# Kernel optimization log

Hardware: AMD Instinct MI355X
Metric: run time of the kernel (lower is better)

The kernel has to match this reference:

```python
import jax, jax.numpy as jnp
import numpy as np

D_CAT = 4096   # number of multinomial categories (input_dim)
HID = 256      # hidden_dim
B = 4096       # batch_size (eta is a (B, D_CAT-1) parameter)
INIT = 1e-3
LOG2PI = float(np.log(2.0 * np.pi))


def _helmert_basis(d):
    """Orthonormal ILR balance basis, shape (d-1, d): rows sum to 0, Psi @ Psi.T = I."""
    i = np.arange(1, d, dtype=np.float64)
    scale = np.sqrt(i / (i + 1.0))
    Psi = np.zeros((d - 1, d), dtype=np.float64)
    tri = np.tril(np.ones((d - 1, d - 1), dtype=np.float64))
    Psi[:, : d - 1] = tri * (scale / i)[:, None]
    Psi[np.arange(d - 1), np.arange(1, d)] = -scale
    return Psi.astype(np.float32)


def setup_inputs() -> dict:
    key = jax.random.key(0)
    k1, k2, k3, k4 = jax.random.split(key, 4)
    n = D_CAT - 1
    x = jax.random.randint(k1, (B, D_CAT), 0, 20).astype(jnp.float32)  # count data
    Psi = jnp.asarray(_helmert_basis(D_CAT))                            # (n, D)
    enc_W = jax.random.normal(k2, (HID, n), dtype=jnp.float32) * INIT   # encoder Linear weight
    dec_W = jax.random.normal(k3, (n, HID), dtype=jnp.float32) * INIT   # decoder Linear weight
    variational_logvars = jnp.zeros((HID,), jnp.float32)
    log_sigma_sq = jnp.float32(0.01)
    eta = jax.random.normal(k4, (B, n), dtype=jnp.float32) * INIT       # learned eta parameter
    return dict(x=x, Psi=Psi, enc_W=enc_W, dec_W=dec_W,
                variational_logvars=variational_logvars,
                log_sigma_sq=log_sigma_sq, eta=eta)


def reference(x, Psi, enc_W, dec_W, variational_logvars, log_sigma_sq, eta):
    # --- ILR transform of imputed counts: clr(log(x+1)) @ Psi^T ---
    logp = jnp.log(x + 1.0)                                   # imputer: x + 1
    clr = logp - logp.mean(-1, keepdims=True)                 # (B, D)
    hx = clr @ Psi.T                                          # (B, n)
    z_mean = hx @ enc_W.T                                     # (B, k)
    mu = z_mean @ dec_W.T                                     # (B, n)

    # --- MultivariateNormalFactorIdentity log_prob via Woodbury / det lemma ---
    # Sigma = var * I_n + W diag(Dv) W^T,  W = dec_W (n, k)
    Dv = jnp.exp(variational_logvars)                         # (k,)
    var = jnp.exp(log_sigma_sq)                               # scalar
    n = dec_W.shape[0]
    WtW = dec_W.T @ dec_W                                     # (k, k)
    M = jnp.diag(1.0 / Dv) + WtW / var                        # capacitance matrix (k, k)
    d = eta - mu                                              # (B, n)
    dW = d @ dec_W                                            # (B, k)
    sol = jnp.linalg.solve(M, dW.T).T                         # (B, k)
    quad = jnp.sum(d * d, -1) / var - jnp.sum(dW * sol, -1) / (var * var)
    _, logdetM = jnp.linalg.slogdet(M)
    logdet_sigma = n * log_sigma_sq + jnp.sum(variational_logvars) + logdetM
    logit_loss = jnp.mean(-0.5 * (n * LOG2PI + logdet_sigma + quad))

    # --- standard-normal prior on z_mean ---
    prior_loss = jnp.mean(-0.5 * z_mean * z_mean - 0.5 * LOG2PI)

    # --- Multinomial log-likelihood with logits = ilr_inv(eta) = eta @ Psi ---
    logits = eta @ Psi                                        # (B, D)
    logsm = jax.nn.log_softmax(logits, -1)
    ntot = x.sum(-1)
    mult = (jax.lax.lgamma(ntot + 1.0)
            - jnp.sum(jax.lax.lgamma(x + 1.0), -1)
            + jnp.sum(x * logsm, -1))
    mult_loss = jnp.mean(mult)

    return -(mult_loss + logit_loss + prior_loss)
```

## Files before the change

### kernel.cpp

```cpp
#include <hip/hip_runtime.h>
#include <math.h>

static constexpr int DC  = 4096;
static constexpr int NM1 = 4095;
static constexpr int HID = 256;
static constexpr int BB  = 4096;
static constexpr double LOG2PI_D = 1.8378770664093454835;

typedef __attribute__((ext_vector_type(8))) __bf16 bf16x8;
typedef __attribute__((ext_vector_type(4))) __bf16 bf16x4;
typedef __attribute__((ext_vector_type(2))) __bf16 bf16x2;
typedef __attribute__((ext_vector_type(4))) float  f32x4;

__device__ __forceinline__ void async16(const __bf16* g, __bf16* l) {
    __builtin_amdgcn_global_load_lds(
        (const __attribute__((address_space(1))) void*)g,
        (__attribute__((address_space(3))) void*)l, 16, 0, 0);
}

__global__ __launch_bounds__(256) void k_pre(
    const float* __restrict__ decW, const float* __restrict__ Psi,
    const float* __restrict__ lv, const float* __restrict__ lss,
    __bf16* __restrict__ decWT, float* __restrict__ av, float* __restrict__ bv,
    float* __restrict__ Dv, float* __restrict__ scal)
{
    __shared__ float tp[32][33];
    const int t = threadIdx.x;
    const int blk = blockIdx.x;
    if (blk < 1024) {
        int bx = blk & 7, by = blk >> 3;
        int tx = t & 31, ty = t >> 5;
        int r0 = by * 32, c0 = bx * 32;
        #pragma unroll
        for (int i = 0; i < 4; i++) {
            int r = r0 + ty + i * 8, c = c0 + tx;
            tp[ty + i * 8][tx] = (r < NM1 && c < HID) ? decW[(size_t)r * HID + c] : 0.f;
        }
        __syncthreads();
        #pragma unroll
        for (int i = 0; i < 4; i++) {
            int c = c0 + ty + i * 8, r = r0 + tx;
            decWT[(size_t)c * DC + r] = (__bf16)tp[tx][ty + i * 8];
        }
    } else if (blk < 1040) {
        int r = (blk - 1024) * 256 + t;
        if (r < NM1) {
            av[r] = Psi[(size_t)r * DC];
            bv[r] = -Psi[(size_t)r * DC + r + 1];
        } else { av[r] = 0.f; bv[r] = 0.f; }
    } else {
        float v = lv[t];
        Dv[t] = expf(v);
        for (int o = 32; o > 0; o >>= 1) v += __shfl_down(v, o);
        __shared__ float red[4];
        if ((t & 63) == 0) red[t >> 6] = v;
        __syncthreads();
        if (t == 0) {
            scal[0] = expf(lss[0]);
            scal[1] = red[0] + red[1] + red[2] + red[3];
        }
    }
}

__global__ __launch_bounds__(256, 6) void k_mega(
    const float* __restrict__ x, const float* __restrict__ eta,
    const float* __restrict__ encW, const __bf16* __restrict__ decWT,
    const float* __restrict__ av, const float* __restrict__ bv,
    float* __restrict__ multv, float* __restrict__ eta2,
    __bf16* __restrict__ clrB, __bf16* __restrict__ etaB,
    __bf16* __restrict__ encPsiB, float* __restrict__ WtW)
{
    __shared__ float smemf[2392];
    const int t = threadIdx.x;
    const int blk = blockIdx.x;
    const int lane = t & 63, w = t >> 6;

    if (blk >= 64 + HID) {
        __bf16* es    = (__bf16*)smemf;
        float* red    = smemf + 2048;
        float* wsumE  = smemf + 2064;
        float* wsumX  = smemf + 2068;
        float* firstX = smemf + 2072;
        float* lutL   = smemf + 2328;
        float* lutG   = smemf + 2360;
        const int b = blk - (64 + HID);
        const int j0 = t * 16;

        const float4* xrow = (const float4*)(x + (size_t)b * DC + j0);
        float4 xq[4];
        #pragma unroll
        for (int i = 0; i < 4; i++) xq[i] = xrow[i];

        const float* erow = eta + (size_t)b * NM1;
        float ee[16];
        #pragma unroll
        for (int i = 0; i < 16; i++) { int j = i * 256 + t; ee[i] = (j < NM1) ? erow[j] : 0.f; }

        if (t < 32) { float f = (float)t + 1.f; lutL[t] = logf(f); lutG[t] = lgammaf(f); }
        __syncthreads();

        bf16x8 xp0, xp1;
        float s = 0.f, slg = 0.f, slp = 0.f;
        {
            float xv[16];
            #pragma unroll
            for (int i = 0; i < 4; i++) {
                xv[i * 4 + 0] = xq[i].x; xv[i * 4 + 1] = xq[i].y;
                xv[i * 4 + 2] = xq[i].z; xv[i * 4 + 3] = xq[i].w;
            }
            #pragma unroll
            for (int i = 0; i < 16; i++) {
                float vf = xv[i];
                int iv = (int)vf;
                float l, g;
                if (vf == (float)iv && iv >= 0 && iv < 32) { l = lutL[iv]; g = lutG[iv]; }
                else { l = logf(vf + 1.f); g = lgammaf(vf + 1.f); }
                s += vf; slg += g; slp += l;
            }
            #pragma unroll
            for (int i = 0; i < 8; i++) { xp0[i] = (__bf16)xv[i]; xp1[i] = (__bf16)xv[i + 8]; }
            firstX[t] = xv[0];
        }
        float e2 = 0.f;
        #pragma unroll
        for (int i = 0; i < 16; i++) {
            float e = ee[i];
            e2 += e * e;
            es[i * 256 + t] = (__bf16)e;
        }
        for (int o = 32; o > 0; o >>= 1) {
            s += __shfl_down(s, o); slg += __shfl_down(slg, o);
            slp += __shfl_down(slp, o); e2 += __shfl_down(e2, o);
        }
        if (lane == 0) { red[w] = s; red[4 + w] = slg; red[8 + w] = slp; red[12 + w] = e2; }
        __syncthreads();

        const float ntotv  = red[0] + red[1] + red[2] + red[3];
        const float sumlgv = red[4] + red[5] + red[6] + red[7];
        const float m = (red[8] + red[9] + red[10] + red[11]) * (1.f / DC);

        {
            bf16x8 c0, c1;
            #pragma unroll
            for (int i = 0; i < 16; i++) {
                float vf = (i < 8) ? (float)xp0[i & 7] : (float)xp1[i & 7];
                int iv = (int)vf;
                float l = (vf == (float)iv && iv >= 0 && iv < 32) ? lutL[iv] : logf(vf + 1.f);
                if (i < 8) c0[i & 7] = (__bf16)(l - m); else c1[i & 7] = (__bf16)(l - m);
            }
            *(bf16x8*)(clrB + (size_t)b * DC + j0)     = c0;
            *(bf16x8*)(clrB + (size_t)b * DC + j0 + 8) = c1;
        }

        bf16x8 e0 = *(const bf16x8*)(es + j0);
        bf16x8 e1 = *(const bf16x8*)(es + j0 + 8);
        *(bf16x8*)(etaB + (size_t)b * DC + j0)     = e0;
        *(bf16x8*)(etaB + (size_t)b * DC + j0 + 8) = e1;

        float avc[16], bvc[16];
        #pragma unroll
        for (int i = 0; i < 16; i += 4) {
            float4 a4 = *(const float4*)(av + j0 + i);
            avc[i] = a4.x; avc[i + 1] = a4.y; avc[i + 2] = a4.z; avc[i + 3] = a4.w;
            float4 b4 = *(const float4*)(bv + j0 + i);
            bvc[i] = b4.x; bvc[i + 1] = b4.y; bvc[i + 2] = b4.z; bvc[i + 3] = b4.w;
        }

        float localE = 0.f, localX = 0.f;
        #pragma unroll
        for (int i = 0; i < 16; i++) {
            float evi = (i < 8) ? (float)e0[i & 7] : (float)e1[i & 7];
            float xvi = (i < 8) ? (float)xp0[i & 7] : (float)xp1[i & 7];
            localE += evi * avc[i]; localX += xvi;
        }
        float incE = localE, incX = localX;
        #pragma unroll
        for (int o = 1; o < 64; o <<= 1) {
            float vE = __shfl_up(incE, o), vX = __shfl_up(incX, o);
            if (lane >= o) { incE += vE; incX += vX; }
        }
        if (lane == 63) { wsumE[w] = incE; wsumX[w] = incX; }
        float eprev = (t > 0) ? (float)es[j0 - 1] : 0.f;
        float bprev = (t > 0) ? bv[j0 - 1] : 0.f;
        float xnl   = (t < 255) ? firstX[t + 1] : 0.f;
        __syncthreads();

        float woffE = 0.f, woffX = 0.f;
        for (int i = 0; i < w; i++) { woffE += wsumE[i]; woffX += wsumX[i]; }
        const float U = wsumE[0] + wsumE[1] + wsumE[2] + wsumE[3];
        float runE = woffE + incE - localE;
        float Xrun = woffX + incX - localX;

        float se = 0.f, sx = 0.f;
        float pE = eprev, pB = bprev;
        #pragma unroll
        for (int i = 0; i < 16; i++) {
            float evi = (i < 8) ? (float)e0[i & 7] : (float)e1[i & 7];
            float xvi = (i < 8) ? (float)xp0[i & 7] : (float)xp1[i & 7];
            float Tj = U - runE;
            runE += evi * avc[i];
            float pw = pE * pB;
            float l = Tj - pw;
            se += expf(l);
            Xrun += xvi;
            float xn = (i < 15) ? ((i + 1 < 8) ? (float)xp0[(i + 1) & 7] : (float)xp1[(i + 1) & 7]) : xnl;
            sx += evi * (avc[i] * Xrun - bvc[i] * xn);
            pE = evi; pB = bvc[i];
        }
        for (int o = 32; o > 0; o >>= 1) {
            se += __shfl_down(se, o); sx += __shfl_down(sx, o);
        }
        if (lane == 0) { red[0 + w] = se; red[4 + w] = sx; }
        __syncthreads();
        if (t == 0) {
            float S1t = red[0] + red[1] + red[2] + red[3];
            float S2t = red[4] + red[5] + red[6] + red[7];
            float e2t = red[12] + red[13] + red[14] + red[15];
            double mult = (double)lgammaf(ntotv + 1.f) - (double)sumlgv
                        + (double)S2t - (double)ntotv * (double)logf(S1t);
            multv[b] = (float)mult;
            eta2[b]  = e2t;
        }
    } else if (blk >= 64) {
        __bf16* es   = (__bf16*)smemf;
        float* wsumE = smemf + 2048;
        const int h = blk - 64;
        const float* erow = encW + (size_t)h * NM1;
        {
            float ee[16];
            #pragma unroll
            for (int i = 0; i < 16; i++) { int j = i * 256 + t; ee[i] = (j < NM1) ? erow[j] : 0.f; }
            #pragma unroll
            for (int i = 0; i < 16; i++) es[i * 256 + t] = (__bf16)ee[i];
        }
        const int j0 = t * 16;
        float avc[16], bvc[16];
        #pragma unroll
        for (int i = 0; i < 16; i += 4) {
            float4 a4 = *(const float4*)(av + j0 + i);
            avc[i] = a4.x; avc[i + 1] = a4.y; avc[i + 2] = a4.z; avc[i + 3] = a4.w;
            float4 b4 = *(const float4*)(bv + j0 + i);
            bvc[i] = b4.x; bvc[i + 1] = b4.y; bvc[i + 2] = b4.z; bvc[i + 3] = b4.w;
        }
        __syncthreads();
        bf16x8 e0 = *(const bf16x8*)(es + j0);
        bf16x8 e1 = *(const bf16x8*)(es + j0 + 8);
        float localE = 0.f;
        #pragma unroll
        for (int i = 0; i < 16; i++) {
            float evi = (i < 8) ? (float)e0[i & 7] : (float)e1[i & 7];
            localE += evi * avc[i];
        }
        float incE = localE;
        #pragma unroll
        for (int o = 1; o < 64; o <<= 1) { float vE = __shfl_up(incE, o); if (lane >= o) incE += vE; }
        if (lane == 63) wsumE[w] = incE;
        float eprev = (t > 0) ? (float)es[j0 - 1] : 0.f;
        float bprev = (t > 0) ? bv[j0 - 1] : 0.f;
        __syncthreads();
        float woffE = 0.f;
        for (int i = 0; i < w; i++) woffE += wsumE[i];
        const float U = wsumE[0] + wsumE[1] + wsumE[2] + wsumE[3];
        float runE = woffE + incE - localE;
        bf16x8 o0, o1;
        float pE = eprev, pB = bprev;
        #pragma unroll
        for (int i = 0; i < 16; i++) {
            float evi = (i < 8) ? (float)e0[i & 7] : (float)e1[i & 7];
            float Tj = U - runE;
            runE += evi * avc[i];
            float pw = pE * pB;
            float l = Tj - pw;
            if (i < 8) o0[i & 7] = (__bf16)l; else o1[i & 7] = (__bf16)l;
            pE = evi; pB = bvc[i];
        }
        *(bf16x8*)(encPsiB + (size_t)h * DC + j0)     = o0;
        *(bf16x8*)(encPsiB + (size_t)h * DC + j0 + 8) = o1;
    } else {
        __bf16* As = (__bf16*)smemf;
        __bf16* Bs = (__bf16*)(smemf + 1024);
        const int w2 = blk;
        const int mn = w2 & 15, sl = w2 >> 4;
        const int m0 = (mn >> 2) * 64, n0 = (mn & 3) * 64, kb = sl * 1024;
        const int ln = lane & 15, q = lane >> 4;
        const int wm = w >> 1, wn = w & 1;
        f32x4 acc[2][2] = {};
        for (int k0 = kb; k0 < kb + 1024; k0 += 32) {
            async16(decWT + (size_t)(m0 + (t >> 2)) * DC + k0 + (t & 3) * 8, As + t * 8);
            async16(decWT + (size_t)(n0 + (t >> 2)) * DC + k0 + (t & 3) * 8, Bs + t * 8);
            __syncthreads();
            bf16x8 af[2], bfr[2];
            #pragma unroll
            for (int i = 0; i < 2; i++) {
                af[i]  = *(const bf16x8*)(As + (wm * 32 + i * 16 + ln) * 32 + q * 8);
                bfr[i] = *(const bf16x8*)(Bs + (wn * 32 + i * 16 + ln) * 32 + q * 8);
            }
            #pragma unroll
            for (int mi = 0; mi < 2; mi++)
                #pragma unroll
                for (int ni = 0; ni < 2; ni++)
                    acc[mi][ni] = __builtin_amdgcn_mfma_f32_16x16x32_bf16(af[mi], bfr[ni], acc[mi][ni], 0, 0, 0);
            __syncthreads();
        }
        #pragma unroll
        for (int mi = 0; mi < 2; mi++)
            #pragma unroll
            for (int rr = 0; rr < 4; rr++) {
                int m = m0 + wm * 32 + mi * 16 + q * 4 + rr;
                #pragma unroll
                for (int ni = 0; ni < 2; ni++)
                    atomicAdd(&WtW[(size_t)m * HID + n0 + wn * 32 + ni * 16 + ln], acc[mi][ni][rr]);
            }
    }
}

__global__ __launch_bounds__(256) void k_combo2(
    const __bf16* __restrict__ clrB, const __bf16* __restrict__ etaB,
    const __bf16* __restrict__ encPsiB, const __bf16* __restrict__ decWT,
    float* __restrict__ part,
    const float* __restrict__ WtW, const float* __restrict__ Dv,
    const float* __restrict__ scal, __bf16* __restrict__ WtWB,
    __bf16* __restrict__ MinvB, float* __restrict__ scal_out)
{
    __shared__ __bf16 As[64 * 64];
    __shared__ __bf16 Bs[256 * 64];
    const int tid = threadIdx.x;
    const int w = tid >> 6, lane = tid & 63;
    const int ln = lane & 15, q = lane >> 4;
    const int wm = w >> 1, wn = w & 1;
    const int bid = blockIdx.x;

    if (bid >= 16) {
        const int idx = bid - 16;
        const int g = idx >> 8, r = idx & 255, sl = r >> 6, mt = r & 63;
        const __bf16* A  = g ? etaB  : clrB;
        const __bf16* Bt = g ? decWT : encPsiB;
        float* C = part + ((size_t)(g * 4 + sl) << 20);
        const int m0 = mt * 64, kb = sl * 1024;
        f32x4 acc[2][8] = {};
        for (int k0 = kb; k0 < kb + 1024; k0 += 64) {
            #pragma unroll
            for (int j = 0; j < 2; j++) {
                int c = j * 256 + tid;
                int row = c >> 3, ch = c & 7;
                async16(A + (size_t)(m0 + row) * DC + k0 + (ch ^ (row & 7)) * 8, As + c * 8);
            }
            #pragma unroll
            for (int j = 0; j < 8; j++) {
                int c = j * 256 + tid;
                int row = c >> 3, ch = c & 7;
                async16(Bt + (size_t)row * DC + k0 + (ch ^ (row & 7)) * 8, Bs + c * 8);
            }
            __syncthreads();
            #pragma unroll
            for (int jj = 0; jj < 2; jj++) {
                bf16x8 af[2], bfr[8];
                #pragma unroll
                for (int i = 0; i < 2; i++) {
                    int arow = wm * 32 + i * 16 + ln;
                    af[i]  = *(const bf16x8*)(As + arow * 64 + ((jj * 4 + q) ^ (arow & 7)) * 8);
                }
                #pragma unroll
                for (int i = 0; i < 8; i++) {
                    int brow = wn * 128 + i * 16 + ln;
                    bfr[i] = *(const bf16x8*)(Bs + brow * 64 + ((jj * 4 + q) ^ (brow & 7)) * 8);
                }
                #pragma unroll
                for (int mi = 0; mi < 2; mi++)
                    #pragma unroll
                    for (int ni = 0; ni < 8; ni++)
                        acc[mi][ni] = __builtin_amdgcn_mfma_f32_16x16x32_bf16(af[mi], bfr[ni], acc[mi][ni], 0, 0, 0);
            }
            __syncthreads();
        }
        #pragma unroll
        for (int mi = 0; mi < 2; mi++)
            #pragma unroll
            for (int rr = 0; rr < 4; rr++) {
                int m = m0 + wm * 32 + mi * 16 + q * 4 + rr;
                #pragma unroll
                for (int ni = 0; ni < 8; ni++) {
                    int n = wn * 128 + ni * 16 + ln;
                    C[(size_t)m * HID + n] = acc[mi][ni][rr];
                }
            }
    } else {
        __shared__ float dvs[HID];
        __shared__ float redc[8];
        const int w2 = bid;
        const int m0 = (w2 >> 2) * 64, n0 = (w2 & 3) * 64;
        dvs[tid] = Dv[tid];
        __syncthreads();
        const float rv = 1.f / scal[0];
        f32x4 acc[2][2] = {};
        for (int k0 = 0; k0 < HID; k0 += 32) {
            {
                int row = tid >> 2, kc = tid & 3;
                const float* srcA = WtW + (size_t)(m0 + row) * HID + k0 + kc * 8;
                const float* srcB = WtW + (size_t)(n0 + row) * HID + k0 + kc * 8;
                float sA = dvs[m0 + row] * rv;
                bf16x8 a8, b8;
                #pragma unroll
                for (int u = 0; u < 8; u++) {
                    a8[u] = (__bf16)(srcA[u] * sA);
                    b8[u] = (__bf16)(srcB[u] * dvs[k0 + kc * 8 + u] * rv);
                }
                *(bf16x8*)(As + tid * 8) = a8;
                *(bf16x8*)(Bs + tid * 8) = b8;
            }
            __syncthreads();
            bf16x8 af[2], bfr[2];
            #pragma unroll
            for (int i = 0; i < 2; i++) {
                af[i]  = *(const bf16x8*)(As + (wm * 32 + i * 16 + ln) * 32 + q * 8);
                bfr[i] = *(const bf16x8*)(Bs + (wn * 32 + i * 16 + ln) * 32 + q * 8);
            }
            #pragma unroll
            for (int mi = 0; mi < 2; mi++)
                #pragma unroll
                for (int ni = 0; ni < 2; ni++)
                    acc[mi][ni] = __builtin_amdgcn_mfma_f32_16x16x32_bf16(af[mi], bfr[ni], acc[mi][ni], 0, 0, 0);
            __syncthreads();
        }
        float t1p = 0.f, t2p = 0.f;
        #pragma unroll
        for (int mi = 0; mi < 2; mi++)
            #pragma unroll
            for (int rr = 0; rr < 4; rr++) {
                int m = m0 + wm * 32 + mi * 16 + q * 4 + rr;
                #pragma unroll
                for (int ni = 0; ni < 2; ni++) {
                    int n = n0 + wn * 32 + ni * 16 + ln;
                    float wmn = WtW[(size_t)m * HID + n];
                    float Bmn = dvs[m] * wmn * rv;
                    float Bnm = dvs[n] * wmn * rv;
                    float mv = (((m == n) ? 1.f : 0.f) - Bmn + acc[mi][ni][rr]) * dvs[n];
                    MinvB[(size_t)m * HID + n] = (__bf16)mv;
                    WtWB[(size_t)m * HID + n] = (__bf16)wmn;
                    t2p += Bmn * Bnm;
                    if (m == n) t1p += Bmn;
                }
            }
        for (int o = 32; o > 0; o >>= 1) { t1p += __shfl_down(t1p, o); t2p += __shfl_down(t2p, o); }
        if (lane == 0) { redc[w] = t1p; redc[4 + w] = t2p; }
        __syncthreads();
        if (tid == 0) {
            atomicAdd(&scal_out[2], redc[0] + redc[1] + redc[2] + redc[3]);
            atomicAdd(&scal_out[3], redc[4] + redc[5] + redc[6] + redc[7]);
        }
    }
}

__global__ __launch_bounds__(256) void mfma_quad(
    const float* __restrict__ part,
    const __bf16* __restrict__ WtWB, const __bf16* __restrict__ MinvB,
    float* __restrict__ r0a, float* __restrict__ r1a, float* __restrict__ r2a,
    float* __restrict__ r3a)
{
    __shared__ __bf16 As[16 * 32];
    __shared__ __bf16 Bs[256 * 32];
    __shared__ __bf16 dWs[16 * 264];
    const int tid = threadIdx.x;
    const int w = tid >> 6, lane = tid & 63;
    const int ln = lane & 15, q = lane >> 4;
    const int m0 = blockIdx.x * 16;
    const float* zp = part;
    const float* ep = part + ((size_t)4 << 20);
    const size_t SL = (size_t)1 << 20;

    f32x4 acc[4] = {};
    for (int k0 = 0; k0 < HID; k0 += 32) {
        {
            int row = tid >> 4, kc = tid & 15;
            size_t off = (size_t)(m0 + row) * HID + k0 + kc * 2;
            float2 v0 = *(const float2*)(zp + off);
            float2 v1 = *(const float2*)(zp + SL + off);
            float2 v2 = *(const float2*)(zp + 2 * SL + off);
            float2 v3 = *(const float2*)(zp + 3 * SL + off);
            float vx = v0.x + v1.x + v2.x + v3.x;
            float vy = v0.y + v1.y + v2.y + v3.y;
            bf16x2 b2 = {(__bf16)vx, (__bf16)vy};
            int ch = kc >> 2, wi = kc & 3;
            *(bf16x2*)(As + row * 32 + ((ch ^ ((row >> 1) & 3)) * 8) + wi * 2) = b2;
        }
        #pragma unroll
        for (int j = 0; j < 4; j++) {
            int c = j * 256 + tid;
            int row = c >> 2, ch = c & 3;
            async16(WtWB + (size_t)row * HID + k0 + (ch ^ ((row >> 1) & 3)) * 8, Bs + c * 8);
        }
        __syncthreads();
        bf16x8 af = *(const bf16x8*)(As + ln * 32 + ((q ^ ((ln >> 1) & 3)) * 8));
        #pragma unroll
        for (int ni = 0; ni < 4; ni++) {
            int brow = w * 64 + ni * 16 + ln;
            bf16x8 bfr = *(const bf16x8*)(Bs + brow * 32 + ((q ^ ((ln >> 1) & 3)) * 8));
            acc[ni] = __builtin_amdgcn_mfma_f32_16x16x32_bf16(af, bfr, acc[ni], 0, 0, 0);
        }
        __syncthreads();
    }
    #pragma unroll
    for (int rr = 0; rr < 4; rr++) {
        int lm = q * 4 + rr;
        int m = m0 + lm;
        float s0 = 0.f, s1 = 0.f, s3 = 0.f;
        #pragma unroll
        for (int ni = 0; ni < 4; ni++) {
            int n = w * 64 + ni * 16 + ln;
            size_t o2 = (size_t)m * HID + n;
            float zv = zp[o2] + zp[SL + o2] + zp[2 * SL + o2] + zp[3 * SL + o2];
            float ew = ep[o2] + ep[SL + o2] + ep[2 * SL + o2] + ep[3 * SL + o2];
            float dv = ew - acc[ni][rr];
            dWs[lm * 264 + n] = (__bf16)dv;
            s0 += ew * zv; s1 += dv * zv; s3 += zv * zv;
        }
        #pragma unroll
        for (int o = 1; o < 16; o <<= 1) {
            s0 += __shfl_xor(s0, o); s1 += __shfl_xor(s1, o); s3 += __shfl_xor(s3, o);
        }
        if (ln == 0) {
            atomicAdd(&r0a[m], s0); atomicAdd(&r1a[m], s1); atomicAdd(&r3a[m], s3);
        }
    }

    f32x4 acc2[4] = {};
    for (int k0 = 0; k0 < HID; k0 += 32) {
        #pragma unroll
        for (int j = 0; j < 4; j++) {
            int c = j * 256 + tid;
            int row = c >> 2, ch = c & 3;
            async16(MinvB + (size_t)row * HID + k0 + (ch ^ ((row >> 1) & 3)) * 8, Bs + c * 8);
        }
        __syncthreads();
        bf16x8 af = *(const bf16x8*)(dWs + ln * 264 + k0 + q * 8);
        #pragma unroll
        for (int ni = 0; ni < 4; ni++) {
            int brow = w * 64 + ni * 16 + ln;
            bf16x8 bfr = *(const bf16x8*)(Bs + brow * 32 + ((q ^ ((ln >> 1) & 3)) * 8));
            acc2[ni] = __builtin_amdgcn_mfma_f32_16x16x32_bf16(af, bfr, acc2[ni], 0, 0, 0);
        }
        __syncthreads();
    }
    #pragma unroll
    for (int rr = 0; rr < 4; rr++) {
        int lm = q * 4 + rr;
        int m = m0 + lm;
        float s2 = 0.f;
        #pragma unroll
        for (int ni = 0; ni < 4; ni++) {
            int n = w * 64 + ni * 16 + ln;
            s2 += (float)dWs[lm * 264 + n] * acc2[ni][rr];
        }
        #pragma unroll
        for (int o = 1; o < 16; o <<= 1) s2 += __shfl_xor(s2, o);
        if (ln == 0) atomicAdd(&r2a[m], s2);
    }
}

__global__ void k_final(const float* __restrict__ multv, const float* __restrict__ eta2,
                        const float* __restrict__ r0a, const float* __restrict__ r1a,
                        const float* __restrict__ r2a, const float* __restrict__ r3a,
                        const float* __restrict__ scal, const float* __restrict__ lss,
                        float* __restrict__ out) {
    int t = threadIdx.x;
    float var = scal[0];
    float rv = 1.f / var;
    double am = 0.0, aq = 0.0, az = 0.0;
    for (int b = t; b < BB; b += 256) {
        am += (double)multv[b];
        aq += (double)((eta2[b] - r0a[b] - r1a[b]) * rv - r2a[b] * rv * rv);
        az += (double)r3a[b];
    }
    for (int o = 32; o > 0; o >>= 1) {
        am += __shfl_down(am, o); aq += __shfl_down(aq, o); az += __shfl_down(az, o);
    }
    __shared__ double red[3][4];
    if ((t & 63) == 0) { int w = t >> 6; red[0][w] = am; red[1][w] = aq; red[2][w] = az; }
    __syncthreads();
    if (t == 0) {
        double mm = (red[0][0] + red[0][1] + red[0][2] + red[0][3]) / (double)BB;
        double mq = (red[1][0] + red[1][1] + red[1][2] + red[1][3]) / (double)BB;
        double mz = (red[2][0] + red[2][1] + red[2][2] + red[2][3]) / ((double)BB * (double)HID);
        double t1 = scal[2], t2 = scal[3];
        double logdetIB = t1 - t2 * 0.5;
        double sumlv = (double)scal[1];
        double logdetM = -sumlv + logdetIB;
        double logdet_sigma = (double)NM1 * (double)lss[0] + sumlv + logdetM;
        double logit_loss = -0.5 * ((double)NM1 * LOG2PI_D + logdet_sigma + mq);
        double prior_loss = -0.5 * mz - 0.5 * LOG2PI_D;
        out[0] = (float)(-(mm + logit_loss + prior_loss));
    }
}


extern "C" void kernel_launch(void* const* d_in, const int* in_sizes, int n_in,
                              void* d_out, int out_size, void* d_ws, size_t ws_size,
                              hipStream_t stream) {
    (void)in_sizes; (void)n_in; (void)out_size; (void)ws_size;
    const float* x    = (const float*)d_in[0];
    const float* Psi  = (const float*)d_in[1];
    const float* encW = (const float*)d_in[2];
    const float* decW = (const float*)d_in[3];
    const float* lv   = (const float*)d_in[4];
    const float* lss  = (const float*)d_in[5];
    const float* eta  = (const float*)d_in[6];
    float* out = (float*)d_out;

    float* wp = (float*)d_ws;
    float* part   = wp;
    float* WtW    = part + ((size_t)8 << 20);
    float* r0a    = WtW    + 65536;
    float* r1a    = r0a    + 4096;
    float* r2a    = r1a    + 4096;
    float* r3a    = r2a    + 4096;
    float* scal   = r3a    + 4096;
    float* av     = scal   + 16;
    float* bv     = av     + 4096;
    float* multv  = bv     + 4096;
    float* eta2   = multv  + 4096;
    float* Dv     = eta2   + 4096;
    __bf16* clrB    = (__bf16*)(Dv + 256);
    __bf16* etaB    = clrB    + (1 << 24);
    __bf16* encPsiB = etaB    + (1 << 24);
    __bf16* decWT   = encPsiB + (1 << 20);
    __bf16* WtWB    = decWT   + (1 << 20);
    __bf16* MinvB   = WtWB    + 65536;

    hipMemsetAsync(WtW, 0, (size_t)(65536 + 4 * 4096 + 16) * sizeof(float), stream);

    k_pre<<<1041, 256, 0, stream>>>(decW, Psi, lv, lss, decWT, av, bv, Dv, scal);

    k_mega<<<64 + HID + BB, 256, 0, stream>>>(x, eta, encW, decWT, av, bv,
                                              multv, eta2, clrB, etaB, encPsiB, WtW);

    k_combo2<<<528, 256, 0, stream>>>(clrB, etaB, encPsiB, decWT, part,
                                      WtW, Dv, scal, WtWB, MinvB, scal);

    mfma_quad<<<256, 256, 0, stream>>>(part, WtWB, MinvB, r0a, r1a, r2a, r3a);

    k_final<<<1, 256, 0, stream>>>(multv, eta2, r0a, r1a, r2a, r3a, scal, lss, out);
}
```

Baseline: 302.9 us.

## Split WtW GEMM out of mega kernel and trim register pressure in row kernel

Moves the WtW MFMA split-K computation into its own kernel with 256 blocks (K slice 256 instead of 1024), leaving the row kernel to handle only encoder-Psi and per-batch rows. The row kernel's launch bound is raised to 8 waves per SIMD, and the bv loads, reduction reads and neighbour values are deferred to where they are used so fewer registers stay live. The aim is higher occupancy for the memory-bound row work and a shorter WtW critical path. The trade-off is an extra kernel launch, and more atomics on WtW because there are more K slices.

```diff
diff --git a/kernel.cpp b/kernel.cpp
--- a/kernel.cpp
+++ b/kernel.cpp
@@ -62,28 +62,69 @@
     }
 }
 
-__global__ __launch_bounds__(256, 6) void k_mega(
+__global__ __launch_bounds__(256) void k_wtw(
+    const __bf16* __restrict__ decWT, float* __restrict__ WtW)
+{
+    __shared__ __bf16 As[64 * 32];
+    __shared__ __bf16 Bs[64 * 32];
+    const int t = threadIdx.x;
+    const int lane = t & 63, w = t >> 6;
+    const int blk = blockIdx.x;
+    const int mn = blk & 15, sl = blk >> 4;
+    const int m0 = (mn >> 2) * 64, n0 = (mn & 3) * 64, kb = sl * 256;
+    const int ln = lane & 15, q = lane >> 4;
+    const int wm = w >> 1, wn = w & 1;
+    f32x4 acc[2][2] = {};
+    for (int k0 = kb; k0 < kb + 256; k0 += 32) {
+        async16(decWT + (size_t)(m0 + (t >> 2)) * DC + k0 + (t & 3) * 8, As + t * 8);
+        async16(decWT + (size_t)(n0 + (t >> 2)) * DC + k0 + (t & 3) * 8, Bs + t * 8);
+        __syncthreads();
+        bf16x8 af[2], bfr[2];
+        #pragma unroll
+        for (int i = 0; i < 2; i++) {
+            af[i]  = *(const bf16x8*)(As + (wm * 32 + i * 16 + ln) * 32 + q * 8);
+            bfr[i] = *(const bf16x8*)(Bs + (wn * 32 + i * 16 + ln) * 32 + q * 8);
+        }
+        #pragma unroll
+        for (int mi = 0; mi < 2; mi++)
+            #pragma unroll
+            for (int ni = 0; ni < 2; ni++)
+                acc[mi][ni] = __builtin_amdgcn_mfma_f32_16x16x32_bf16(af[mi], bfr[ni], acc[mi][ni], 0, 0, 0);
+        __syncthreads();
+    }
+    #pragma unroll
+    for (int mi = 0; mi < 2; mi++)
+        #pragma unroll
+        for (int rr = 0; rr < 4; rr++) {
+            int m = m0 + wm * 32 + mi * 16 + q * 4 + rr;
+            #pragma unroll
+            for (int ni = 0; ni < 2; ni++)
+                atomicAdd(&WtW[(size_t)m * HID + n0 + wn * 32 + ni * 16 + ln], acc[mi][ni][rr]);
+        }
+}
+
+__global__ __launch_bounds__(256, 8) void k_rows(
     const float* __restrict__ x, const float* __restrict__ eta,
-    const float* __restrict__ encW, const __bf16* __restrict__ decWT,
+    const float* __restrict__ encW,
     const float* __restrict__ av, const float* __restrict__ bv,
     float* __restrict__ multv, float* __restrict__ eta2,
     __bf16* __restrict__ clrB, __bf16* __restrict__ etaB,
-    __bf16* __restrict__ encPsiB, float* __restrict__ WtW)
+    __bf16* __restrict__ encPsiB)
 {
-    __shared__ float smemf[2392];
+    __shared__ float smemf[2400];
     const int t = threadIdx.x;
     const int blk = blockIdx.x;
     const int lane = t & 63, w = t >> 6;
 
-    if (blk >= 64 + HID) {
+    if (blk >= 256) {
         __bf16* es    = (__bf16*)smemf;
         float* red    = smemf + 2048;
-        float* wsumE  = smemf + 2064;
-        float* wsumX  = smemf + 2068;
-        float* firstX = smemf + 2072;
-        float* lutL   = smemf + 2328;
-        float* lutG   = smemf + 2360;
-        const int b = blk - (64 + HID);
+        float* wsumE  = smemf + 2072;
+        float* wsumX  = smemf + 2076;
+        float* firstX = smemf + 2080;
+        float* lutL   = smemf + 2336;
+        float* lutG   = smemf + 2368;
+        const int b = blk - 256;
         const int j0 = t * 16;
 
         const float4* xrow = (const float4*)(x + (size_t)b * DC + j0);
@@ -135,11 +176,8 @@
         if (lane == 0) { red[w] = s; red[4 + w] = slg; red[8 + w] = slp; red[12 + w] = e2; }
         __syncthreads();
 
-        const float ntotv  = red[0] + red[1] + red[2] + red[3];
-        const float sumlgv = red[4] + red[5] + red[6] + red[7];
-        const float m = (red[8] + red[9] + red[10] + red[11]) * (1.f / DC);
-
         {
+            const float m = (red[8] + red[9] + red[10] + red[11]) * (1.f / DC);
             bf16x8 c0, c1;
             #pragma unroll
             for (int i = 0; i < 16; i++) {
@@ -157,13 +195,11 @@
         *(bf16x8*)(etaB + (size_t)b * DC + j0)     = e0;
         *(bf16x8*)(etaB + (size_t)b * DC + j0 + 8) = e1;
 
-        float avc[16], bvc[16];
+        float avc[16];
         #pragma unroll
         for (int i = 0; i < 16; i += 4) {
             float4 a4 = *(const float4*)(av + j0 + i);
             avc[i] = a4.x; avc[i + 1] = a4.y; avc[i + 2] = a4.z; avc[i + 3] = a4.w;
-            float4 b4 = *(const float4*)(bv + j0 + i);
-            bvc[i] = b4.x; bvc[i + 1] = b4.y; bvc[i + 2] = b4.z; bvc[i + 3] = b4.w;
         }
 
         float localE = 0.f, localX = 0.f;
@@ -180,9 +216,6 @@
             if (lane >= o) { incE += vE; incX += vX; }
         }
         if (lane == 63) { wsumE[w] = incE; wsumX[w] = incX; }
-        float eprev = (t > 0) ? (float)es[j0 - 1] : 0.f;
-        float bprev = (t > 0) ? bv[j0 - 1] : 0.f;
-        float xnl   = (t < 255) ? firstX[t + 1] : 0.f;
         __syncthreads();
 
         float woffE = 0.f, woffX = 0.f;
@@ -190,6 +223,16 @@
         const float U = wsumE[0] + wsumE[1] + wsumE[2] + wsumE[3];
         float runE = woffE + incE - localE;
         float Xrun = woffX + incX - localX;
+
+        float eprev = (t > 0) ? (float)es[j0 - 1] : 0.f;
+        float bprev = (t > 0) ? bv[j0 - 1] : 0.f;
+        float xnl   = (t < 255) ? firstX[t + 1] : 0.f;
+        float bvc[16];
+        #pragma unroll
+        for (int i = 0; i < 16; i += 4) {
+            float4 b4 = *(const float4*)(bv + j0 + i);
+            bvc[i] = b4.x; bvc[i + 1] = b4.y; bvc[i + 2] = b4.z; bvc[i + 3] = b4.w;
+        }
 
         float se = 0.f, sx = 0.f;
         float pE = eprev, pB = bprev;
@@ -210,21 +253,23 @@
         for (int o = 32; o > 0; o >>= 1) {
             se += __shfl_down(se, o); sx += __shfl_down(sx, o);
         }
-        if (lane == 0) { red[0 + w] = se; red[4 + w] = sx; }
+        if (lane == 0) { red[16 + w] = se; red[20 + w] = sx; }
         __syncthreads();
         if (t == 0) {
-            float S1t = red[0] + red[1] + red[2] + red[3];
-            float S2t = red[4] + red[5] + red[6] + red[7];
+            float ntotv  = red[0] + red[1] + red[2] + red[3];
+            float sumlgv = red[4] + red[5] + red[6] + red[7];
+            float S1t = red[16] + red[17] + red[18] + red[19];
+            float S2t = red[20] + red[21] + red[22] + red[23];
             float e2t = red[12] + red[13] + red[14] + red[15];
             double mult = (double)lgammaf(ntotv + 1.f) - (double)sumlgv
                         + (double)S2t - (double)ntotv * (double)logf(S1t);
             multv[b] = (float)mult;
             eta2[b]  = e2t;
         }
-    } else if (blk >= 64) {
+    } else {
         __bf16* es   = (__bf16*)smemf;
         float* wsumE = smemf + 2048;
-        const int h = blk - 64;
+        const int h = blk;
         const float* erow = encW + (size_t)h * NM1;
         {
             float ee[16];
@@ -234,13 +279,11 @@
             for (int i = 0; i < 16; i++) es[i * 256 + t] = (__bf16)ee[i];
         }
         const int j0 = t * 16;
-        float avc[16], bvc[16];
+        float avc[16];
         #pragma unroll
         for (int i = 0; i < 16; i += 4) {
             float4 a4 = *(const float4*)(av + j0 + i);
             avc[i] = a4.x; avc[i + 1] = a4.y; avc[i + 2] = a4.z; avc[i + 3] = a4.w;
-            float4 b4 = *(const float4*)(bv + j0 + i);
-            bvc[i] = b4.x; bvc[i + 1] = b4.y; bvc[i + 2] = b4.z; bvc[i + 3] = b4.w;
         }
         __syncthreads();
         bf16x8 e0 = *(const bf16x8*)(es + j0);
@@ -255,13 +298,19 @@
         #pragma unroll
         for (int o = 1; o < 64; o <<= 1) { float vE = __shfl_up(incE, o); if (lane >= o) incE += vE; }
         if (lane == 63) wsumE[w] = incE;
-        float eprev = (t > 0) ? (float)es[j0 - 1] : 0.f;
-        float bprev = (t > 0) ? bv[j0 - 1] : 0.f;
         __syncthreads();
         float woffE = 0.f;
         for (int i = 0; i < w; i++) woffE += wsumE[i];
         const float U = wsumE[0] + wsumE[1] + wsumE[2] + wsumE[3];
         float runE = woffE + incE - localE;
+        float eprev = (t > 0) ? (float)es[j0 - 1] : 0.f;
+        float bprev = (t > 0) ? bv[j0 - 1] : 0.f;
+        float bvc[16];
+        #pragma unroll
+        for (int i = 0; i < 16; i += 4) {
+            float4 b4 = *(const float4*)(bv + j0 + i);
+            bvc[i] = b4.x; bvc[i + 1] = b4.y; bvc[i + 2] = b4.z; bvc[i + 3] = b4.w;
+        }
         bf16x8 o0, o1;
         float pE = eprev, pB = bprev;
         #pragma unroll
@@ -276,41 +325,6 @@
         }
         *(bf16x8*)(encPsiB + (size_t)h * DC + j0)     = o0;
         *(bf16x8*)(encPsiB + (size_t)h * DC + j0 + 8) = o1;
-    } else {
-        __bf16* As = (__bf16*)smemf;
-        __bf16* Bs = (__bf16*)(smemf + 1024);
-        const int w2 = blk;
-        const int mn = w2 & 15, sl = w2 >> 4;
-        const int m0 = (mn >> 2) * 64, n0 = (mn & 3) * 64, kb = sl * 1024;
-        const int ln = lane & 15, q = lane >> 4;
-        const int wm = w >> 1, wn = w & 1;
-        f32x4 acc[2][2] = {};
-        for (int k0 = kb; k0 < kb + 1024; k0 += 32) {
-            async16(decWT + (size_t)(m0 + (t >> 2)) * DC + k0 + (t & 3) * 8, As + t * 8);
-            async16(decWT + (size_t)(n0 + (t >> 2)) * DC + k0 + (t & 3) * 8, Bs + t * 8);
-            __syncthreads();
-            bf16x8 af[2], bfr[2];
-            #pragma unroll
-            for (int i = 0; i < 2; i++) {
-                af[i]  = *(const bf16x8*)(As + (wm * 32 + i * 16 + ln) * 32 + q * 8);
-                bfr[i] = *(const bf16x8*)(Bs + (wn * 32 + i * 16 + ln) * 32 + q * 8);
-            }
-            #pragma unroll
-            for (int mi = 0; mi < 2; mi++)
-                #pragma unroll
-                for (int ni = 0; ni < 2; ni++)
-                    acc[mi][ni] = __builtin_amdgcn_mfma_f32_16x16x32_bf16(af[mi], bfr[ni], acc[mi][ni], 0, 0, 0);
-            __syncthreads();
-        }
-        #pragma unroll
-        for (int mi = 0; mi < 2; mi++)
-            #pragma unroll
-            for (int rr = 0; rr < 4; rr++) {
-                int m = m0 + wm * 32 + mi * 16 + q * 4 + rr;
-                #pragma unroll
-                for (int ni = 0; ni < 2; ni++)
-                    atomicAdd(&WtW[(size_t)m * HID + n0 + wn * 32 + ni * 16 + ln], acc[mi][ni][rr]);
-            }
     }
 }
 
@@ -630,8 +644,10 @@
 
     k_pre<<<1041, 256, 0, stream>>>(decW, Psi, lv, lss, decWT, av, bv, Dv, scal);
 
-    k_mega<<<64 + HID + BB, 256, 0, stream>>>(x, eta, encW, decWT, av, bv,
-                                              multv, eta2, clrB, etaB, encPsiB, WtW);
+    k_wtw<<<256, 256, 0, stream>>>(decWT, WtW);
+
+    k_rows<<<256 + BB, 256, 0, stream>>>(x, eta, encW, av, bv,
+                                         multv, eta2, clrB, etaB, encPsiB);
 
     k_combo2<<<528, 256, 0, stream>>>(clrB, etaB, encPsiB, decWT, part,
                                       WtW, Dv, scal, WtWB, MinvB, scal);
```

After: 333.6 us. 10.1% more time.
